# Kernel optimization log

Measured on AMD Instinct MI355X. Metric: run time of the kernel, lower is better.

## Reference

```python
import jax, jax.numpy as jnp
import numpy as np

DIM = 1024
DIM_INNER = 2048
B, S = 4, 4096


def setup_inputs() -> dict:
    key = jax.random.key(0)
    k1, k2, k3 = jax.random.split(key, 3)
    x = jax.random.normal(k1, (B, S, DIM), dtype=jnp.float32)
    # torch Linear weight init ~ U(-1/sqrt(fan_in), 1/sqrt(fan_in)); scaled normals are fine
    W_hg = jax.random.normal(k2, (DIM, 2 * DIM_INNER), dtype=jnp.float32) / np.sqrt(DIM)
    W_out = jax.random.normal(k3, (DIM_INNER, DIM), dtype=jnp.float32) / np.sqrt(DIM_INNER)
    return {"x": x, "W_hg": W_hg, "W_out": W_out}


def heinsen_associative_scan_log(log_coeffs, log_values):
    # a_star[t] = sum_{i<=t} log_coeffs[i]
    a_star = jnp.cumsum(log_coeffs, axis=1)
    log_h0_plus_b_star = jax.lax.cumlogsumexp(log_values - a_star, axis=1)
    return jnp.exp(a_star + log_h0_plus_b_star)


def reference(x, W_hg, W_out):
    # fused projection then split into hidden / gate, each [B, S, DIM_INNER]
    hg = jnp.einsum('bsd,de->bse', x, W_hg)
    hidden, gate = jnp.split(hg, 2, axis=-1)
    # seq_len > 1, prev_hidden = None path of the torch module
    log_z = jax.nn.log_sigmoid(gate)                 # log sigmoid(gate)
    log_coeffs = -jax.nn.softplus(gate)              # log(1 - sigmoid(gate))
    hidden_log = jnp.log(jax.nn.relu(hidden) + 0.5)  # log(g(hidden)) as coded (relu+0.5)
    log_values = hidden_log + log_z
    h = heinsen_associative_scan_log(log_coeffs, log_values)  # [B, S, DIM_INNER]
    out = jnp.einsum('bse,ed->bsd', h, W_out)
    return out
```

## Files before the change

kernel.cpp:

```cpp
#include <hip/hip_runtime.h>
#include <stdint.h>

#define DIMX 1024
#define DIM_INNER 2048
#define BATCH 4
#define SEQ 4096
#define M_TOTAL (BATCH * SEQ)
#define N_HG (2 * DIM_INNER)
#define NCHUNK 256
#define CLEN 16

typedef unsigned short u16;
typedef __attribute__((ext_vector_type(8))) short short8;
typedef __attribute__((ext_vector_type(4))) float floatx4;

__device__ __forceinline__ float bflo(uint32_t u) { return __uint_as_float(u << 16); }
__device__ __forceinline__ float bfhi(uint32_t u) { return __uint_as_float(u & 0xffff0000u); }
__device__ __forceinline__ uint32_t f2bf_bits(float f) {
    uint32_t u = __float_as_uint(f);
    return (u + 0x7fffu + ((u >> 16) & 1u)) >> 16;
}

__global__ __launch_bounds__(256) void prep(const float* __restrict__ x,
                                            const float* __restrict__ Whg,
                                            const float* __restrict__ Wout,
                                            u16* __restrict__ xb,
                                            u16* __restrict__ whgt,
                                            u16* __restrict__ woutt) {
    __shared__ float tile[64][65];
    const int bid = blockIdx.x;
    const int tid = threadIdx.x;
    if (bid < 2048) {
        const int n4 = M_TOTAL * DIMX / 4;
        const float4* in4 = (const float4*)x;
        ushort4* out4 = (ushort4*)xb;
        for (int i = bid * 256 + tid; i < n4; i += 2048 * 256) {
            float4 v = in4[i];
            ushort4 o;
            o.x = (u16)f2bf_bits(v.x);
            o.y = (u16)f2bf_bits(v.y);
            o.z = (u16)f2bf_bits(v.z);
            o.w = (u16)f2bf_bits(v.w);
            out4[i] = o;
        }
        return;
    }
    const float* in;
    u16* out;
    int R, C, tb;
    if (bid < 3072) {
        in = Whg; out = whgt; R = DIMX; C = N_HG; tb = bid - 2048;
    } else {
        in = Wout; out = woutt; R = DIM_INNER; C = DIMX; tb = bid - 3072;
    }
    const int tilesx = C / 64;
    const int c0 = (tb % tilesx) * 64, r0 = (tb / tilesx) * 64;
    const int tx = tid & 63, ty = tid >> 6;
#pragma unroll
    for (int i = ty; i < 64; i += 4)
        tile[i][tx] = in[(size_t)(r0 + i) * C + c0 + tx];
    __syncthreads();
#pragma unroll
    for (int i = ty; i < 64; i += 4)
        out[(size_t)(c0 + i) * R + r0 + tx] = (u16)f2bf_bits(tile[tx][i]);
}

template <int OUT_BF16>
__global__ __launch_bounds__(256, 2) void gemm_bf16(const u16* __restrict__ A,
                                                    const u16* __restrict__ Bt,
                                                    void* __restrict__ C,
                                                    const int M, const int N, const int K) {
    __shared__ alignas(16) u16 As[128 * 32];
    __shared__ alignas(16) u16 Bs[128 * 32];

    const int tid = threadIdx.x;
    const int lane = tid & 63;
    const int wave = tid >> 6;
    const int wm = (wave >> 1) * 64;
    const int wn = (wave & 1) * 64;
    const size_t m0 = (size_t)blockIdx.y * 128;
    const size_t n0 = (size_t)blockIdx.x * 128;

    floatx4 acc[4][4];
#pragma unroll
    for (int i = 0; i < 4; ++i)
#pragma unroll
        for (int j = 0; j < 4; ++j) acc[i][j] = (floatx4){0.f, 0.f, 0.f, 0.f};

    const int srow = lane >> 2;
    const int scol = ((lane & 3) ^ ((srow >> 1) & 3)) * 8;
    const u16* Ag = A + m0 * K + (size_t)(wave * 16 + srow) * K + scol;
    const u16* Bg = Bt + n0 * K + (size_t)(wave * 16 + srow) * K + scol;
    u16* Asw = As + (wave * 16) * 32;
    u16* Bsw = Bs + (wave * 16) * 32;

    const int fr = lane & 15;
    const int kblk = lane >> 4;
    const int koff = (kblk ^ ((fr >> 1) & 3)) * 8;

    for (int k0 = 0; k0 < K; k0 += 32) {
        __syncthreads();
#pragma unroll
        for (int i = 0; i < 2; ++i) {
            __builtin_amdgcn_global_load_lds(
                (const __attribute__((address_space(1))) uint32_t*)(const void*)(Ag + (size_t)i * 64 * K + k0),
                (__attribute__((address_space(3))) uint32_t*)(void*)(Asw + i * 64 * 32),
                16, 0, 0);
            __builtin_amdgcn_global_load_lds(
                (const __attribute__((address_space(1))) uint32_t*)(const void*)(Bg + (size_t)i * 64 * K + k0),
                (__attribute__((address_space(3))) uint32_t*)(void*)(Bsw + i * 64 * 32),
                16, 0, 0);
        }
        __syncthreads();

        short8 af[4], bfr[4];
#pragma unroll
        for (int i = 0; i < 4; ++i)
            af[i] = *(const short8*)(As + (wm + i * 16 + fr) * 32 + koff);
#pragma unroll
        for (int j = 0; j < 4; ++j)
            bfr[j] = *(const short8*)(Bs + (wn + j * 16 + fr) * 32 + koff);
#pragma unroll
        for (int i = 0; i < 4; ++i)
#pragma unroll
            for (int j = 0; j < 4; ++j)
                acc[i][j] = __builtin_amdgcn_mfma_f32_16x16x32_bf16(af[i], bfr[j], acc[i][j], 0, 0, 0);
    }

    const int r0row = (lane >> 4) * 4;
#pragma unroll
    for (int i = 0; i < 4; ++i) {
#pragma unroll
        for (int r = 0; r < 4; ++r) {
            size_t row = m0 + wm + i * 16 + r0row + r;
#pragma unroll
            for (int j = 0; j < 4; ++j) {
                size_t col = n0 + wn + j * 16 + fr;
                float v = acc[i][j][r];
                if (OUT_BF16)
                    ((u16*)C)[row * N + col] = (u16)f2bf_bits(v);
                else
                    ((float*)C)[row * N + col] = v;
            }
        }
    }
}

__device__ __forceinline__ void av_pair(uint32_t hh, uint32_t gg,
                                        float& a0, float& v0, float& a1, float& v1) {
    float h0 = bflo(hh), h1 = bfhi(hh);
    float g0 = bflo(gg), g1 = bfhi(gg);
    g0 = fminf(fmaxf(g0, -30.f), 30.f);
    g1 = fminf(fmaxf(g1, -30.f), 30.f);
    float e0 = __expf(-g0), e1 = __expf(-g1);
    float z0 = 1.f / (1.f + e0), z1 = 1.f / (1.f + e1);
    a0 = e0 * z0;
    a1 = e1 * z1;
    v0 = z0 * (fmaxf(h0, 0.f) + 0.5f);
    v1 = z1 * (fmaxf(h1, 0.f) + 0.5f);
}

__device__ __forceinline__ void av8(uint4 hh, uint4 gg, float* a, float* v) {
    av_pair(hh.x, gg.x, a[0], v[0], a[1], v[1]);
    av_pair(hh.y, gg.y, a[2], v[2], a[3], v[3]);
    av_pair(hh.z, gg.z, a[4], v[4], a[5], v[5]);
    av_pair(hh.w, gg.w, a[6], v[6], a[7], v[7]);
}

__global__ __launch_bounds__(256) void scan_chunks(const u16* __restrict__ hg,
                                                   float2* __restrict__ sumAV) {
    const int b = blockIdx.y, ch = blockIdx.x;
    const int c8 = threadIdx.x * 8;
    const size_t rowbase = (size_t)b * SEQ + (size_t)ch * CLEN;
    const u16* p = hg + rowbase * 4096 + c8;
    float A[8], V[8];
#pragma unroll
    for (int k = 0; k < 8; ++k) { A[k] = 1.f; V[k] = 0.f; }
    uint4 h0 = *(const uint4*)(p);
    uint4 g0 = *(const uint4*)(p + 2048);
    uint4 h1 = *(const uint4*)(p + 4096);
    uint4 g1 = *(const uint4*)(p + 4096 + 2048);
#pragma unroll 4
    for (int j = 0; j < CLEN; ++j) {
        uint4 h2, g2;
        if (j + 2 < CLEN) {
            h2 = *(const uint4*)(p + (size_t)(j + 2) * 4096);
            g2 = *(const uint4*)(p + (size_t)(j + 2) * 4096 + 2048);
        }
        float a[8], v[8];
        av8(h0, g0, a, v);
#pragma unroll
        for (int k = 0; k < 8; ++k) { V[k] = fmaf(a[k], V[k], v[k]); A[k] *= a[k]; }
        h0 = h1; g0 = g1; h1 = h2; g1 = g2;
    }
    float4* dst = (float4*)(sumAV + (size_t)(b * NCHUNK + ch) * 2048 + c8);
    dst[0] = (float4){A[0], V[0], A[1], V[1]};
    dst[1] = (float4){A[2], V[2], A[3], V[3]};
    dst[2] = (float4){A[4], V[4], A[5], V[5]};
    dst[3] = (float4){A[6], V[6], A[7], V[7]};
}

__global__ __launch_bounds__(64) void scan_carry(const float2* __restrict__ sumAV,
                                                 float* __restrict__ carry) {
    const int g = blockIdx.x * 64 + threadIdx.x;
    const int b = g >> 11, c = g & 2047;
    float h = 0.f;
#pragma unroll 8
    for (int ch = 0; ch < NCHUNK; ++ch) {
        float2 s = sumAV[(size_t)(b * NCHUNK + ch) * 2048 + c];
        carry[(size_t)(b * NCHUNK + ch) * 2048 + c] = h;
        h = fmaf(s.x, h, s.y);
    }
}

__global__ __launch_bounds__(256) void scan_apply(const u16* __restrict__ hg,
                                                  const float* __restrict__ carry,
                                                  uint32_t* __restrict__ hbuf) {
    const int b = blockIdx.y, ch = blockIdx.x;
    const int c8 = threadIdx.x * 8;
    const size_t rowbase = (size_t)b * SEQ + (size_t)ch * CLEN;
    const u16* p = hg + rowbase * 4096 + c8;
    uint32_t* q = hbuf + rowbase * 1024 + c8 / 2;
    const float4* cin = (const float4*)(carry + (size_t)(b * NCHUNK + ch) * 2048 + c8);
    float4 cl = cin[0], chh = cin[1];
    float H[8] = {cl.x, cl.y, cl.z, cl.w, chh.x, chh.y, chh.z, chh.w};
    uint4 h0 = *(const uint4*)(p);
    uint4 g0 = *(const uint4*)(p + 2048);
    uint4 h1 = *(const uint4*)(p + 4096);
    uint4 g1 = *(const uint4*)(p + 4096 + 2048);
#pragma unroll 4
    for (int j = 0; j < CLEN; ++j) {
        uint4 h2, g2;
        if (j + 2 < CLEN) {
            h2 = *(const uint4*)(p + (size_t)(j + 2) * 4096);
            g2 = *(const uint4*)(p + (size_t)(j + 2) * 4096 + 2048);
        }
        float a[8], v[8];
        av8(h0, g0, a, v);
#pragma unroll
        for (int k = 0; k < 8; ++k) H[k] = fmaf(a[k], H[k], v[k]);
        uint4 o;
        o.x = f2bf_bits(H[0]) | (f2bf_bits(H[1]) << 16);
        o.y = f2bf_bits(H[2]) | (f2bf_bits(H[3]) << 16);
        o.z = f2bf_bits(H[4]) | (f2bf_bits(H[5]) << 16);
        o.w = f2bf_bits(H[6]) | (f2bf_bits(H[7]) << 16);
        *(uint4*)(q + (size_t)j * 1024) = o;
        h0 = h1; g0 = g1; h1 = h2; g1 = g2;
    }
}

extern "C" void kernel_launch(void* const* d_in, const int* in_sizes, int n_in,
                              void* d_out, int out_size, void* d_ws, size_t ws_size,
                              hipStream_t stream) {
    const float* x = (const float*)d_in[0];
    const float* Whg = (const float*)d_in[1];
    const float* Wout = (const float*)d_in[2];

    char* ws = (char*)d_ws;
    size_t off = 0;
    u16* xb = (u16*)(ws + off);        off += (size_t)M_TOTAL * DIMX * 2;
    u16* whgt = (u16*)(ws + off);      off += (size_t)N_HG * DIMX * 2;
    u16* woutt = (u16*)(ws + off);     off += (size_t)DIMX * DIM_INNER * 2;
    u16* hg = (u16*)(ws + off);        off += (size_t)M_TOTAL * N_HG * 2;
    uint32_t* hbuf = (uint32_t*)(ws + off); off += (size_t)M_TOTAL * DIM_INNER * 2;
    float2* sumAV = (float2*)(ws + 0);
    float* carry = (float*)(ws + (size_t)BATCH * NCHUNK * DIM_INNER * 8);

    prep<<<2048 + 1024 + 512, 256, 0, stream>>>(x, Whg, Wout, xb, whgt, woutt);

    gemm_bf16<1><<<dim3(N_HG / 128, M_TOTAL / 128), 256, 0, stream>>>(xb, whgt, hg, M_TOTAL, N_HG, DIMX);

    scan_chunks<<<dim3(NCHUNK, BATCH), 256, 0, stream>>>(hg, sumAV);
    scan_carry<<<dim3(128), 64, 0, stream>>>(sumAV, carry);
    scan_apply<<<dim3(NCHUNK, BATCH), 256, 0, stream>>>(hg, carry, hbuf);

    gemm_bf16<0><<<dim3(DIMX / 128, M_TOTAL / 128), 256, 0, stream>>>((const u16*)hbuf, woutt, d_out, M_TOTAL, DIMX, DIM_INNER);
}
```

Measured before the change: 461.6 us.

## Fuse gate activation and chunk-scan summary into first GEMM epilogue

After: 421.9 us. 1.09x faster.

```diff
diff --git a/kernel.cpp b/kernel.cpp
--- a/kernel.cpp
+++ b/kernel.cpp
@@ -7,8 +7,8 @@
 #define SEQ 4096
 #define M_TOTAL (BATCH * SEQ)
 #define N_HG (2 * DIM_INNER)
-#define NCHUNK 256
-#define CLEN 16
+#define NCHUNK 32
+#define CLEN 128
 
 typedef unsigned short u16;
 typedef __attribute__((ext_vector_type(8))) short short8;
@@ -65,11 +65,135 @@
         out[(size_t)(c0 + i) * R + r0 + tx] = (u16)f2bf_bits(tile[tx][i]);
 }
 
-template <int OUT_BF16>
-__global__ __launch_bounds__(256, 2) void gemm_bf16(const u16* __restrict__ A,
-                                                    const u16* __restrict__ Bt,
-                                                    void* __restrict__ C,
-                                                    const int M, const int N, const int K) {
+__global__ __launch_bounds__(256, 2) void gemm1_k(const u16* __restrict__ A,
+                                                  const u16* __restrict__ Bt,
+                                                  uint32_t* __restrict__ av,
+                                                  float2* __restrict__ sumAV) {
+    __shared__ alignas(16) char smem[65536];
+    u16* As = (u16*)smem;
+    u16* Bh = (u16*)(smem + 8192);
+    u16* Bg = (u16*)(smem + 16384);
+    uint32_t* avl = (uint32_t*)smem;
+
+    const int tid = threadIdx.x;
+    const int lane = tid & 63;
+    const int wave = tid >> 6;
+    const int wm = (wave >> 1) * 64;
+    const int wn = (wave & 1) * 64;
+    const size_t m0 = (size_t)blockIdx.y * 128;
+    const int n0 = blockIdx.x * 128;
+
+    floatx4 acch[4][4], accg[4][4];
+#pragma unroll
+    for (int i = 0; i < 4; ++i)
+#pragma unroll
+        for (int j = 0; j < 4; ++j) {
+            acch[i][j] = (floatx4){0.f, 0.f, 0.f, 0.f};
+            accg[i][j] = (floatx4){0.f, 0.f, 0.f, 0.f};
+        }
+
+    const int srow = lane >> 2;
+    const int scol = ((lane & 3) ^ ((srow >> 1) & 3)) * 8;
+    const u16* Ag = A + m0 * DIMX + (size_t)(wave * 16 + srow) * DIMX + scol;
+    const u16* Bhg = Bt + (size_t)n0 * DIMX + (size_t)(wave * 16 + srow) * DIMX + scol;
+    const u16* Bgg = Bt + (size_t)(DIM_INNER + n0) * DIMX + (size_t)(wave * 16 + srow) * DIMX + scol;
+    u16* Asw = As + (wave * 16) * 32;
+    u16* Bhw = Bh + (wave * 16) * 32;
+    u16* Bgw = Bg + (wave * 16) * 32;
+
+    const int fr = lane & 15;
+    const int kblk = lane >> 4;
+    const int koff = (kblk ^ ((fr >> 1) & 3)) * 8;
+
+    for (int k0 = 0; k0 < DIMX; k0 += 32) {
+        __syncthreads();
+#pragma unroll
+        for (int i = 0; i < 2; ++i) {
+            __builtin_amdgcn_global_load_lds(
+                (const __attribute__((address_space(1))) uint32_t*)(const void*)(Ag + (size_t)i * 64 * DIMX + k0),
+                (__attribute__((address_space(3))) uint32_t*)(void*)(Asw + i * 64 * 32), 16, 0, 0);
+            __builtin_amdgcn_global_load_lds(
+                (const __attribute__((address_space(1))) uint32_t*)(const void*)(Bhg + (size_t)i * 64 * DIMX + k0),
+                (__attribute__((address_space(3))) uint32_t*)(void*)(Bhw + i * 64 * 32), 16, 0, 0);
+            __builtin_amdgcn_global_load_lds(
+                (const __attribute__((address_space(1))) uint32_t*)(const void*)(Bgg + (size_t)i * 64 * DIMX + k0),
+                (__attribute__((address_space(3))) uint32_t*)(void*)(Bgw + i * 64 * 32), 16, 0, 0);
+        }
+        __syncthreads();
+
+        short8 af[4], bhf[4], bgf[4];
+#pragma unroll
+        for (int i = 0; i < 4; ++i)
+            af[i] = *(const short8*)(As + (wm + i * 16 + fr) * 32 + koff);
+#pragma unroll
+        for (int j = 0; j < 4; ++j) {
+            bhf[j] = *(const short8*)(Bh + (wn + j * 16 + fr) * 32 + koff);
+            bgf[j] = *(const short8*)(Bg + (wn + j * 16 + fr) * 32 + koff);
+        }
+#pragma unroll
+        for (int i = 0; i < 4; ++i)
+#pragma unroll
+            for (int j = 0; j < 4; ++j) {
+                acch[i][j] = __builtin_amdgcn_mfma_f32_16x16x32_bf16(af[i], bhf[j], acch[i][j], 0, 0, 0);
+                accg[i][j] = __builtin_amdgcn_mfma_f32_16x16x32_bf16(af[i], bgf[j], accg[i][j], 0, 0, 0);
+            }
+    }
+    __syncthreads();
+
+    const int r0row = (lane >> 4) * 4;
+#pragma unroll
+    for (int i = 0; i < 4; ++i) {
+#pragma unroll
+        for (int r = 0; r < 4; ++r) {
+            const int row = wm + i * 16 + r0row + r;
+#pragma unroll
+            for (int j = 0; j < 4; ++j) {
+                const int col = wn + j * 16 + fr;
+                float h = acch[i][j][r];
+                float g = accg[i][j][r];
+                g = fminf(fmaxf(g, -30.f), 30.f);
+                float e = __expf(-g);
+                float z = 1.f / (1.f + e);
+                float a = e * z;
+                float v = z * (fmaxf(h, 0.f) + 0.5f);
+                uint32_t pk = f2bf_bits(a) | (f2bf_bits(v) << 16);
+                avl[row * 128 + col] = pk;
+                av[(m0 + row) * 2048 + n0 + col] = pk;
+            }
+        }
+    }
+    __syncthreads();
+
+    const int col = tid & 127;
+    const int rlo = (tid >> 7) * 64;
+    float Aa = 1.f, Vv = 0.f;
+#pragma unroll 8
+    for (int j = 0; j < 64; ++j) {
+        uint32_t pk = avl[(rlo + j) * 128 + col];
+        float a = bflo(pk), v = bfhi(pk);
+        Vv = fmaf(a, Vv, v);
+        Aa *= a;
+    }
+    __syncthreads();
+    if (tid < 128) {
+        avl[col] = __float_as_uint(Aa);
+        avl[128 + col] = __float_as_uint(Vv);
+    }
+    __syncthreads();
+    if (tid >= 128) {
+        float Al = __uint_as_float(avl[col]);
+        float Vl = __uint_as_float(avl[128 + col]);
+        float At = Al * Aa;
+        float Vt = fmaf(Aa, Vl, Vv);
+        const int chunk = (int)(m0 >> 7);
+        sumAV[(size_t)chunk * 2048 + n0 + col] = (float2){At, Vt};
+    }
+}
+
+__global__ __launch_bounds__(256, 2) void gemm2_k(const u16* __restrict__ A,
+                                                  const u16* __restrict__ Bt,
+                                                  float* __restrict__ C) {
+    const int M = M_TOTAL, N = DIMX, K = DIM_INNER;
     __shared__ alignas(16) u16 As[128 * 32];
     __shared__ alignas(16) u16 Bs[128 * 32];
 
@@ -104,12 +228,10 @@
         for (int i = 0; i < 2; ++i) {
             __builtin_amdgcn_global_load_lds(
                 (const __attribute__((address_space(1))) uint32_t*)(const void*)(Ag + (size_t)i * 64 * K + k0),
-                (__attribute__((address_space(3))) uint32_t*)(void*)(Asw + i * 64 * 32),
-                16, 0, 0);
+                (__attribute__((address_space(3))) uint32_t*)(void*)(Asw + i * 64 * 32), 16, 0, 0);
             __builtin_amdgcn_global_load_lds(
                 (const __attribute__((address_space(1))) uint32_t*)(const void*)(Bg + (size_t)i * 64 * K + k0),
-                (__attribute__((address_space(3))) uint32_t*)(void*)(Bsw + i * 64 * 32),
-                16, 0, 0);
+                (__attribute__((address_space(3))) uint32_t*)(void*)(Bsw + i * 64 * 32), 16, 0, 0);
         }
         __syncthreads();
 
@@ -129,75 +251,16 @@
 
     const int r0row = (lane >> 4) * 4;
 #pragma unroll
-    for (int i = 0; i < 4; ++i) {
+    for (int i = 0; i < 4; ++i)
 #pragma unroll
         for (int r = 0; r < 4; ++r) {
             size_t row = m0 + wm + i * 16 + r0row + r;
 #pragma unroll
             for (int j = 0; j < 4; ++j) {
                 size_t col = n0 + wn + j * 16 + fr;
-                float v = acc[i][j][r];
-                if (OUT_BF16)
-                    ((u16*)C)[row * N + col] = (u16)f2bf_bits(v);
-                else
-                    ((float*)C)[row * N + col] = v;
+                C[row * N + col] = acc[i][j][r];
             }
         }
-    }
-}
-
-__device__ __forceinline__ void av_pair(uint32_t hh, uint32_t gg,
-                                        float& a0, float& v0, float& a1, float& v1) {
-    float h0 = bflo(hh), h1 = bfhi(hh);
-    float g0 = bflo(gg), g1 = bfhi(gg);
-    g0 = fminf(fmaxf(g0, -30.f), 30.f);
-    g1 = fminf(fmaxf(g1, -30.f), 30.f);
-    float e0 = __expf(-g0), e1 = __expf(-g1);
-    float z0 = 1.f / (1.f + e0), z1 = 1.f / (1.f + e1);
-    a0 = e0 * z0;
-    a1 = e1 * z1;
-    v0 = z0 * (fmaxf(h0, 0.f) + 0.5f);
-    v1 = z1 * (fmaxf(h1, 0.f) + 0.5f);
-}
-
-__device__ __forceinline__ void av8(uint4 hh, uint4 gg, float* a, float* v) {
-    av_pair(hh.x, gg.x, a[0], v[0], a[1], v[1]);
-    av_pair(hh.y, gg.y, a[2], v[2], a[3], v[3]);
-    av_pair(hh.z, gg.z, a[4], v[4], a[5], v[5]);
-    av_pair(hh.w, gg.w, a[6], v[6], a[7], v[7]);
-}
-
-__global__ __launch_bounds__(256) void scan_chunks(const u16* __restrict__ hg,
-                                                   float2* __restrict__ sumAV) {
-    const int b = blockIdx.y, ch = blockIdx.x;
-    const int c8 = threadIdx.x * 8;
-    const size_t rowbase = (size_t)b * SEQ + (size_t)ch * CLEN;
-    const u16* p = hg + rowbase * 4096 + c8;
-    float A[8], V[8];
-#pragma unroll
-    for (int k = 0; k < 8; ++k) { A[k] = 1.f; V[k] = 0.f; }
-    uint4 h0 = *(const uint4*)(p);
-    uint4 g0 = *(const uint4*)(p + 2048);
-    uint4 h1 = *(const uint4*)(p + 4096);
-    uint4 g1 = *(const uint4*)(p + 4096 + 2048);
-#pragma unroll 4
-    for (int j = 0; j < CLEN; ++j) {
-        uint4 h2, g2;
-        if (j + 2 < CLEN) {
-            h2 = *(const uint4*)(p + (size_t)(j + 2) * 4096);
-            g2 = *(const uint4*)(p + (size_t)(j + 2) * 4096 + 2048);
-        }
-        float a[8], v[8];
-        av8(h0, g0, a, v);
-#pragma unroll
-        for (int k = 0; k < 8; ++k) { V[k] = fmaf(a[k], V[k], v[k]); A[k] *= a[k]; }
-        h0 = h1; g0 = g1; h1 = h2; g1 = g2;
-    }
-    float4* dst = (float4*)(sumAV + (size_t)(b * NCHUNK + ch) * 2048 + c8);
-    dst[0] = (float4){A[0], V[0], A[1], V[1]};
-    dst[1] = (float4){A[2], V[2], A[3], V[3]};
-    dst[2] = (float4){A[4], V[4], A[5], V[5]};
-    dst[3] = (float4){A[6], V[6], A[7], V[7]};
 }
 
 __global__ __launch_bounds__(64) void scan_carry(const float2* __restrict__ sumAV,
@@ -213,39 +276,29 @@
     }
 }
 
-__global__ __launch_bounds__(256) void scan_apply(const u16* __restrict__ hg,
+__global__ __launch_bounds__(256) void scan_apply(const uint32_t* __restrict__ av,
                                                   const float* __restrict__ carry,
                                                   uint32_t* __restrict__ hbuf) {
-    const int b = blockIdx.y, ch = blockIdx.x;
-    const int c8 = threadIdx.x * 8;
+    const int b = blockIdx.z, ch = blockIdx.y;
+    const int c2 = blockIdx.x * 256 + threadIdx.x;
     const size_t rowbase = (size_t)b * SEQ + (size_t)ch * CLEN;
-    const u16* p = hg + rowbase * 4096 + c8;
-    uint32_t* q = hbuf + rowbase * 1024 + c8 / 2;
-    const float4* cin = (const float4*)(carry + (size_t)(b * NCHUNK + ch) * 2048 + c8);
-    float4 cl = cin[0], chh = cin[1];
-    float H[8] = {cl.x, cl.y, cl.z, cl.w, chh.x, chh.y, chh.z, chh.w};
-    uint4 h0 = *(const uint4*)(p);
-    uint4 g0 = *(const uint4*)(p + 2048);
-    uint4 h1 = *(const uint4*)(p + 4096);
-    uint4 g1 = *(const uint4*)(p + 4096 + 2048);
+    const uint32_t* p = av + rowbase * 2048 + c2 * 2;
+    uint32_t* q = hbuf + rowbase * 1024 + c2;
+    const float2 cin = ((const float2*)carry)[(size_t)(b * NCHUNK + ch) * 1024 + c2];
+    float h0 = cin.x, h1 = cin.y;
+    uint2 p0 = *(const uint2*)(p);
+    uint2 p1 = *(const uint2*)(p + 2048);
 #pragma unroll 4
     for (int j = 0; j < CLEN; ++j) {
-        uint4 h2, g2;
-        if (j + 2 < CLEN) {
-            h2 = *(const uint4*)(p + (size_t)(j + 2) * 4096);
-            g2 = *(const uint4*)(p + (size_t)(j + 2) * 4096 + 2048);
-        }
-        float a[8], v[8];
-        av8(h0, g0, a, v);
-#pragma unroll
-        for (int k = 0; k < 8; ++k) H[k] = fmaf(a[k], H[k], v[k]);
-        uint4 o;
-        o.x = f2bf_bits(H[0]) | (f2bf_bits(H[1]) << 16);
-        o.y = f2bf_bits(H[2]) | (f2bf_bits(H[3]) << 16);
-        o.z = f2bf_bits(H[4]) | (f2bf_bits(H[5]) << 16);
-        o.w = f2bf_bits(H[6]) | (f2bf_bits(H[7]) << 16);
-        *(uint4*)(q + (size_t)j * 1024) = o;
-        h0 = h1; g0 = g1; h1 = h2; g1 = g2;
+        uint2 p2;
+        if (j + 2 < CLEN) p2 = *(const uint2*)(p + (size_t)(j + 2) * 2048);
+        float a0 = bflo(p0.x), v0 = bfhi(p0.x);
+        float a1 = bflo(p0.y), v1 = bfhi(p0.y);
+        h0 = fmaf(a0, h0, v0);
+        h1 = fmaf(a1, h1, v1);
+        q[(size_t)j * 1024] = f2bf_bits(h0) | (f2bf_bits(h1) << 16);
+        p0 = p1;
+        p1 = p2;
     }
 }
 
@@ -261,18 +314,17 @@
     u16* xb = (u16*)(ws + off);        off += (size_t)M_TOTAL * DIMX * 2;
     u16* whgt = (u16*)(ws + off);      off += (size_t)N_HG * DIMX * 2;
     u16* woutt = (u16*)(ws + off);     off += (size_t)DIMX * DIM_INNER * 2;
-    u16* hg = (u16*)(ws + off);        off += (size_t)M_TOTAL * N_HG * 2;
+    uint32_t* av = (uint32_t*)(ws + off); off += (size_t)M_TOTAL * DIM_INNER * 4;
     uint32_t* hbuf = (uint32_t*)(ws + off); off += (size_t)M_TOTAL * DIM_INNER * 2;
-    float2* sumAV = (float2*)(ws + 0);
-    float* carry = (float*)(ws + (size_t)BATCH * NCHUNK * DIM_INNER * 8);
+    float2* sumAV = (float2*)(ws + off); off += (size_t)BATCH * NCHUNK * DIM_INNER * 8;
+    float* carry = (float*)whgt;
 
     prep<<<2048 + 1024 + 512, 256, 0, stream>>>(x, Whg, Wout, xb, whgt, woutt);
 
-    gemm_bf16<1><<<dim3(N_HG / 128, M_TOTAL / 128), 256, 0, stream>>>(xb, whgt, hg, M_TOTAL, N_HG, DIMX);
-
-    scan_chunks<<<dim3(NCHUNK, BATCH), 256, 0, stream>>>(hg, sumAV);
-    scan_carry<<<dim3(128), 64, 0, stream>>>(sumAV, carry);
-    scan_apply<<<dim3(NCHUNK, BATCH), 256, 0, stream>>>(hg, carry, hbuf);
-
-    gemm_bf16<0><<<dim3(DIMX / 128, M_TOTAL / 128), 256, 0, stream>>>((const u16*)hbuf, woutt, d_out, M_TOTAL, DIMX, DIM_INNER);
-}
+    gemm1_k<<<dim3(16, 128), 256, 0, stream>>>(xb, whgt, av, sumAV);
+
+    scan_carry<<<128, 64, 0, stream>>>(sumAV, carry);
+    scan_apply<<<dim3(4, NCHUNK, BATCH), 256, 0, stream>>>(av, carry, hbuf);
+
+    gemm2_k<<<dim3(8, 128), 256, 0, stream>>>((const u16*)hbuf, woutt, (float*)d_out);
+}
```
